# Optimization experiments

Measured on AMD Instinct MI355X. Metric: run time of the kernel, lower is better.

The kernel has to match this reference:

```python
import jax, jax.numpy as jnp
import numpy as np

N_QUBITS = 4
DIM = 2 ** N_QUBITS  # 16
B = 262144
N_FEATURES = 64


def _apply_ry(state, theta, q):
    # state: (B, 16) complex64; theta: scalar or (B,) angle; RY on wire q (wire 0 = MSB)
    b = state.shape[0]
    L, R = 2 ** q, 2 ** (N_QUBITS - 1 - q)
    s = state.reshape(b, L, 2, R)
    theta = jnp.broadcast_to(jnp.asarray(theta, jnp.float32), (b,))
    c = jnp.cos(theta * 0.5)[:, None, None]
    sn = jnp.sin(theta * 0.5)[:, None, None]
    s0, s1 = s[:, :, 0], s[:, :, 1]
    n0 = c * s0 - sn * s1
    n1 = sn * s0 + c * s1
    return jnp.stack([n0, n1], axis=2).reshape(b, DIM)


def _apply_rz(state, theta, q):
    # RZ(theta) = diag(exp(-i theta/2), exp(+i theta/2)) on wire q
    b = state.shape[0]
    L, R = 2 ** q, 2 ** (N_QUBITS - 1 - q)
    s = state.reshape(b, L, 2, R)
    theta = jnp.broadcast_to(jnp.asarray(theta, jnp.float32), (b,))
    p = jnp.exp(-0.5j * theta)[:, None, None].astype(state.dtype)
    n0 = s[:, :, 0] * p
    n1 = s[:, :, 1] * jnp.conj(p)
    return jnp.stack([n0, n1], axis=2).reshape(b, DIM)


def _cnot(state, c):
    # CNOT with control wire c, target wire c+1 (adjacent, as in the circuit)
    b = state.shape[0]
    L, R = 2 ** c, 2 ** (N_QUBITS - 2 - c)
    s = state.reshape(b, L, 2, 2, R)
    s1 = jnp.flip(s[:, :, 1], axis=2)  # flip target when control=1
    return jnp.stack([s[:, :, 0], s1], axis=2).reshape(b, DIM)


def _simulate(angles, w):
    # angles: (B, 4) input RY rotations; w: (8, 2) trainable gate angles
    b = angles.shape[0]
    state = jnp.zeros((b, DIM), jnp.complex64).at[:, 0].set(1.0)
    for q in range(N_QUBITS):
        state = _apply_ry(state, angles[:, q], q)
    for q in range(N_QUBITS):
        state = _apply_rz(state, w[q, 0], q)
        state = _apply_ry(state, w[q, 1], q)
    for q in range(N_QUBITS - 1):
        state = _cnot(state, q)
    for q in range(N_QUBITS):
        state = _apply_rz(state, w[q + N_QUBITS, 0], q)
        state = _apply_ry(state, w[q + N_QUBITS, 1], q)
    probs = (state.real ** 2 + state.imag ** 2).reshape((b,) + (2,) * N_QUBITS)
    outs = []
    for q in range(N_QUBITS):
        axes = tuple(a for a in range(1, N_QUBITS + 1) if a != q + 1)
        p = probs.sum(axis=axes)  # (B, 2)
        outs.append(p[:, 0] - p[:, 1])  # <Z_q>
    return jnp.stack(outs, axis=1).astype(jnp.float32)


def setup_inputs() -> dict:
    key = jax.random.key(0)
    k1, k2, k3 = jax.random.split(key, 3)
    x = jax.random.normal(k1, (B, N_FEATURES), jnp.float32)
    fm_w = jax.random.normal(k2, (N_QUBITS, N_FEATURES), jnp.float32) / jnp.sqrt(N_FEATURES)
    fm_b = jnp.zeros((N_QUBITS,), jnp.float32)
    # TorchLayer default init: uniform(0, 2*pi)
    q_weights = jax.random.uniform(k3, (2 * N_QUBITS, 2), jnp.float32, 0.0, 2.0 * np.pi)
    return {"x": x, "fm_w": fm_w, "fm_b": fm_b, "q_weights": q_weights}


def reference(x, fm_w, fm_b, q_weights):
    angles = x @ fm_w.T + fm_b  # feature_map Linear(n_features -> n_qubits)
    return _simulate(angles, q_weights)  # (B, n_qubits) Pauli-Z expectations
```

## Files before the change

kernel.cpp:

```cpp
#include <hip/hip_runtime.h>

#define NQ 4
#define DIM 16
#define NPAIR 136
#define TPB 512

__global__ __launch_bounds__(TPB, 4) void qnn_fused(
    const float* __restrict__ x, const float* __restrict__ fm_w,
    const float* __restrict__ fm_b, const float* __restrict__ w,
    float* __restrict__ out, int B) {
    __shared__ float Ure[DIM][DIM + 1];
    __shared__ float Uim[DIM][DIM + 1];
    __shared__ float ApackS[NPAIR * 4];

    const int tid = threadIdx.x;

    if ((tid >> 6) == 0) {
        const int lane = tid & 63;
        const int k = lane & 15;
        float sv, cv;
        sincosf(0.5f * w[k], &sv, &cv);
        float sp[16], cp[16];
#pragma unroll
        for (int g = 0; g < 16; ++g) { sp[g] = __shfl(sv, g); cp[g] = __shfl(cv, g); }

#pragma unroll
        for (int cc = 0; cc < 4; ++cc) {
            const int col = (lane >> 4) + 4 * cc;
            float re = (k == col) ? 1.f : 0.f, im = 0.f;
#pragma unroll
            for (int layer = 0; layer < 2; ++layer) {
#pragma unroll
                for (int q = 0; q < NQ; ++q) {
                    const int bit = 1 << (3 - q);
                    const int gz = layer * 8 + q * 2;
                    {
                        const float s = sp[gz], c = cp[gz];
                        const float ssr = (k & bit) ? -s : s;
                        const float nre = re * c + im * ssr;
                        const float nim = im * c - re * ssr;
                        re = nre; im = nim;
                    }
                    {
                        const float s = sp[gz + 1], c = cp[gz + 1];
                        const float pre = __shfl_xor(re, bit);
                        const float pim = __shfl_xor(im, bit);
                        const float se = (k & bit) ? s : -s;
                        re = c * re + se * pre;
                        im = c * im + se * pim;
                    }
                }
                if (layer == 0) {
#pragma unroll
                    for (int c3 = 0; c3 < 3; ++c3) {
                        const int cb = 1 << (3 - c3), tb = 1 << (2 - c3);
                        const float pre = __shfl_xor(re, tb);
                        const float pim = __shfl_xor(im, tb);
                        if (k & cb) { re = pre; im = pim; }
                    }
                }
            }
            Ure[k][col] = re;
            Uim[k][col] = im;
        }
    }
    __syncthreads();

    for (int d = tid; d < NPAIR * 4; d += TPB) {
        const int p = d >> 2, q = d & 3;
        int i = 0, j = 0, pp = p;
        for (i = 0; i < DIM; ++i) {
            const int row = DIM - i;
            if (pp < row) { j = i + pp; break; }
            pp -= row;
        }
        const float f = (i == j) ? 1.f : 2.f;
        float acc = 0.f;
#pragma unroll
        for (int kk = 0; kk < DIM; ++kk) {
            const float zq = ((kk >> (3 - q)) & 1) ? -1.f : 1.f;
            acc += zq * (Ure[kk][i] * Ure[kk][j] + Uim[kk][i] * Uim[kk][j]);
        }
        ApackS[d] = f * acc;
    }
    __syncthreads();

    const long long b = (long long)blockIdx.x * TPB + tid;
    if (b >= B) return;

    float acc[NQ];
#pragma unroll
    for (int q = 0; q < NQ; ++q) acc[q] = fm_b[q];

    const float4* __restrict__ x4 = (const float4*)(x + b * 64);
    const float4* __restrict__ w4 = (const float4*)fm_w;
#pragma unroll
    for (int t = 0; t < 16; ++t) {
        const float4 xv = x4[t];
#pragma unroll
        for (int q = 0; q < NQ; ++q) {
            const float4 wv = w4[q * 16 + t];
            acc[q] += xv.x * wv.x + xv.y * wv.y + xv.z * wv.z + xv.w * wv.w;
        }
    }

    float c[NQ], s[NQ];
#pragma unroll
    for (int q = 0; q < NQ; ++q) __sincosf(0.5f * acc[q], &s[q], &c[q]);

    float p01[4], p23[4];
#pragma unroll
    for (int u = 0; u < 4; ++u) {
        p01[u] = ((u & 2) ? s[0] : c[0]) * ((u & 1) ? s[1] : c[1]);
        p23[u] = ((u & 2) ? s[2] : c[2]) * ((u & 1) ? s[3] : c[3]);
    }
    float st[DIM];
#pragma unroll
    for (int i = 0; i < DIM; ++i) st[i] = p01[i >> 2] * p23[i & 3];

    float o0 = 0.f, o1 = 0.f, o2 = 0.f, o3 = 0.f;
    const float4* __restrict__ A4 = (const float4*)ApackS;
    int p = 0;
#pragma unroll
    for (int i = 0; i < DIM; ++i) {
#pragma unroll
        for (int j = i; j < DIM; ++j) {
            const float pr = st[i] * st[j];
            const float4 aq = A4[p];
            o0 += aq.x * pr; o1 += aq.y * pr; o2 += aq.z * pr; o3 += aq.w * pr;
            ++p;
        }
    }

    *(float4*)(out + b * 4) = make_float4(o0, o1, o2, o3);
}

extern "C" void kernel_launch(void* const* d_in, const int* in_sizes, int n_in,
                              void* d_out, int out_size, void* d_ws, size_t ws_size,
                              hipStream_t stream) {
    const float* x    = (const float*)d_in[0];
    const float* fm_w = (const float*)d_in[1];
    const float* fm_b = (const float*)d_in[2];
    const float* qw   = (const float*)d_in[3];
    float* out = (float*)d_out;

    const int B = in_sizes[0] / 64;

    qnn_fused<<<(B + TPB - 1) / TPB, TPB, 0, stream>>>(x, fm_w, fm_b, qw, out, B);
}
```

Measured before the change: 24.80 us.

## Simulate circuit per thread directly instead of precomputed quadratic-form tables

Removes the per-block shared-memory unitary construction and the 136x4 quadratic-form table, and has each thread apply the RZ/RY/CNOT gates directly on a 16-amplitude register state, then reduce to Pauli-Z expectations. This avoids the block-level setup phase, its two barriers and the LDS reads in the 136-term inner loop, at the cost of more per-thread ALU work, about 16 sincos calls and higher register pressure. Block size also drops from 512 to 256.

```diff
diff --git a/kernel.cpp b/kernel.cpp
--- a/kernel.cpp
+++ b/kernel.cpp
@@ -2,90 +2,50 @@
 
 #define NQ 4
 #define DIM 16
-#define NPAIR 136
-#define TPB 512
+#define TPB 256
+
+
+template <int BIT>
+__device__ __forceinline__ void rz_gate(float* re, float* im, float cz, float sz) {
+#pragma unroll
+    for (int k = 0; k < DIM; ++k) {
+        const float ss = (k & BIT) ? -sz : sz;
+        const float nr = re[k] * cz + im[k] * ss;
+        const float ni = im[k] * cz - re[k] * ss;
+        re[k] = nr; im[k] = ni;
+    }
+}
+
+template <int BIT>
+__device__ __forceinline__ void ry_gate(float* re, float* im, float cy, float sy) {
+#pragma unroll
+    for (int k = 0; k < DIM; ++k) {
+        if (!(k & BIT)) {
+            const int k1 = k | BIT;
+            const float r0 = re[k], i0 = im[k], r1 = re[k1], i1 = im[k1];
+            re[k]  = cy * r0 - sy * r1;  im[k]  = cy * i0 - sy * i1;
+            re[k1] = sy * r0 + cy * r1;  im[k1] = sy * i0 + cy * i1;
+        }
+    }
+}
+
+template <int CB, int TB>
+__device__ __forceinline__ void cnot(float* re, float* im) {
+    float tr[DIM], ti[DIM];
+#pragma unroll
+    for (int k = 0; k < DIM; ++k) {
+        const int ks = (k & CB) ? (k ^ TB) : k;
+        tr[k] = re[ks]; ti[k] = im[ks];
+    }
+#pragma unroll
+    for (int k = 0; k < DIM; ++k) { re[k] = tr[k]; im[k] = ti[k]; }
+}
 
 __global__ __launch_bounds__(TPB, 4) void qnn_fused(
     const float* __restrict__ x, const float* __restrict__ fm_w,
     const float* __restrict__ fm_b, const float* __restrict__ w,
     float* __restrict__ out, int B) {
-    __shared__ float Ure[DIM][DIM + 1];
-    __shared__ float Uim[DIM][DIM + 1];
-    __shared__ float ApackS[NPAIR * 4];
-
-    const int tid = threadIdx.x;
-
-    if ((tid >> 6) == 0) {
-        const int lane = tid & 63;
-        const int k = lane & 15;
-        float sv, cv;
-        sincosf(0.5f * w[k], &sv, &cv);
-        float sp[16], cp[16];
-#pragma unroll
-        for (int g = 0; g < 16; ++g) { sp[g] = __shfl(sv, g); cp[g] = __shfl(cv, g); }
-
-#pragma unroll
-        for (int cc = 0; cc < 4; ++cc) {
-            const int col = (lane >> 4) + 4 * cc;
-            float re = (k == col) ? 1.f : 0.f, im = 0.f;
-#pragma unroll
-            for (int layer = 0; layer < 2; ++layer) {
-#pragma unroll
-                for (int q = 0; q < NQ; ++q) {
-                    const int bit = 1 << (3 - q);
-                    const int gz = layer * 8 + q * 2;
-                    {
-                        const float s = sp[gz], c = cp[gz];
-                        const float ssr = (k & bit) ? -s : s;
-                        const float nre = re * c + im * ssr;
-                        const float nim = im * c - re * ssr;
-                        re = nre; im = nim;
-                    }
-                    {
-                        const float s = sp[gz + 1], c = cp[gz + 1];
-                        const float pre = __shfl_xor(re, bit);
-                        const float pim = __shfl_xor(im, bit);
-                        const float se = (k & bit) ? s : -s;
-                        re = c * re + se * pre;
-                        im = c * im + se * pim;
-                    }
-                }
-                if (layer == 0) {
-#pragma unroll
-                    for (int c3 = 0; c3 < 3; ++c3) {
-                        const int cb = 1 << (3 - c3), tb = 1 << (2 - c3);
-                        const float pre = __shfl_xor(re, tb);
-                        const float pim = __shfl_xor(im, tb);
-                        if (k & cb) { re = pre; im = pim; }
-                    }
-                }
-            }
-            Ure[k][col] = re;
-            Uim[k][col] = im;
-        }
-    }
-    __syncthreads();
-
-    for (int d = tid; d < NPAIR * 4; d += TPB) {
-        const int p = d >> 2, q = d & 3;
-        int i = 0, j = 0, pp = p;
-        for (i = 0; i < DIM; ++i) {
-            const int row = DIM - i;
-            if (pp < row) { j = i + pp; break; }
-            pp -= row;
-        }
-        const float f = (i == j) ? 1.f : 2.f;
-        float acc = 0.f;
-#pragma unroll
-        for (int kk = 0; kk < DIM; ++kk) {
-            const float zq = ((kk >> (3 - q)) & 1) ? -1.f : 1.f;
-            acc += zq * (Ure[kk][i] * Ure[kk][j] + Uim[kk][i] * Uim[kk][j]);
-        }
-        ApackS[d] = f * acc;
-    }
-    __syncthreads();
-
-    const long long b = (long long)blockIdx.x * TPB + tid;
+    const long long b = (long long)blockIdx.x * TPB + threadIdx.x;
     if (b >= B) return;
 
     float acc[NQ];
@@ -118,18 +78,76 @@
 #pragma unroll
     for (int i = 0; i < DIM; ++i) st[i] = p01[i >> 2] * p23[i & 3];
 
+    float re[DIM], im[DIM];
+
+    {
+        float sz, cz; __sincosf(0.5f * w[0], &sz, &cz);
+#pragma unroll
+        for (int k = 0; k < DIM; ++k) {
+            re[k] = st[k] * cz;
+            im[k] = (k & 8) ? st[k] * sz : -(st[k] * sz);
+        }
+    }
+    {
+        float sy, cy; __sincosf(0.5f * w[1], &sy, &cy);
+        ry_gate<8>(re, im, cy, sy);
+    }
+    {
+        float sz, cz; __sincosf(0.5f * w[2], &sz, &cz);
+        rz_gate<4>(re, im, cz, sz);
+        float sy, cy; __sincosf(0.5f * w[3], &sy, &cy);
+        ry_gate<4>(re, im, cy, sy);
+    }
+    {
+        float sz, cz; __sincosf(0.5f * w[4], &sz, &cz);
+        rz_gate<2>(re, im, cz, sz);
+        float sy, cy; __sincosf(0.5f * w[5], &sy, &cy);
+        ry_gate<2>(re, im, cy, sy);
+    }
+    {
+        float sz, cz; __sincosf(0.5f * w[6], &sz, &cz);
+        rz_gate<1>(re, im, cz, sz);
+        float sy, cy; __sincosf(0.5f * w[7], &sy, &cy);
+        ry_gate<1>(re, im, cy, sy);
+    }
+
+    cnot<8, 4>(re, im);
+    cnot<4, 2>(re, im);
+    cnot<2, 1>(re, im);
+
+    {
+        float sz, cz; __sincosf(0.5f * w[8], &sz, &cz);
+        rz_gate<8>(re, im, cz, sz);
+        float sy, cy; __sincosf(0.5f * w[9], &sy, &cy);
+        ry_gate<8>(re, im, cy, sy);
+    }
+    {
+        float sz, cz; __sincosf(0.5f * w[10], &sz, &cz);
+        rz_gate<4>(re, im, cz, sz);
+        float sy, cy; __sincosf(0.5f * w[11], &sy, &cy);
+        ry_gate<4>(re, im, cy, sy);
+    }
+    {
+        float sz, cz; __sincosf(0.5f * w[12], &sz, &cz);
+        rz_gate<2>(re, im, cz, sz);
+        float sy, cy; __sincosf(0.5f * w[13], &sy, &cy);
+        ry_gate<2>(re, im, cy, sy);
+    }
+    {
+        float sz, cz; __sincosf(0.5f * w[14], &sz, &cz);
+        rz_gate<1>(re, im, cz, sz);
+        float sy, cy; __sincosf(0.5f * w[15], &sy, &cy);
+        ry_gate<1>(re, im, cy, sy);
+    }
+
     float o0 = 0.f, o1 = 0.f, o2 = 0.f, o3 = 0.f;
-    const float4* __restrict__ A4 = (const float4*)ApackS;
-    int p = 0;
 #pragma unroll
-    for (int i = 0; i < DIM; ++i) {
-#pragma unroll
-        for (int j = i; j < DIM; ++j) {
-            const float pr = st[i] * st[j];
-            const float4 aq = A4[p];
-            o0 += aq.x * pr; o1 += aq.y * pr; o2 += aq.z * pr; o3 += aq.w * pr;
-            ++p;
-        }
+    for (int k = 0; k < DIM; ++k) {
+        const float pk = re[k] * re[k] + im[k] * im[k];
+        o0 += (k & 8) ? -pk : pk;
+        o1 += (k & 4) ? -pk : pk;
+        o2 += (k & 2) ? -pk : pk;
+        o3 += (k & 1) ? -pk : pk;
     }
 
     *(float4*)(out + b * 4) = make_float4(o0, o1, o2, o3);
```

After: 24.86 us. No clear change (+0.2%).
